# Performance work log

Measured on AMD Instinct MI355X. Metric: run time of the kernel, lower is better.

Reference implementation:

```python
import jax, jax.numpy as jnp
import numpy as np

T, B, C, H, W = 9, 8, 256, 56, 56


def setup_inputs() -> dict:
    key = jax.random.key(0)
    k1, k2, k3, k4 = jax.random.split(key, 4)
    feature_maps_sequence = jax.random.normal(k1, (T, B, C, H, W), dtype=jnp.float32)
    # Conv2d(2C, 1, kernel_size=1): weight [1, 2C, 1, 1], bias [1]
    w = jax.random.normal(k2, (1, 2 * C, 1, 1), dtype=jnp.float32) * 0.02
    b = jax.random.normal(k3, (1,), dtype=jnp.float32) * 0.02
    gamma = jax.random.normal(k4, (1,), dtype=jnp.float32)
    return {"feature_maps_sequence": feature_maps_sequence, "w": w, "b": b, "gamma": gamma}


def reference(feature_maps_sequence, w, b, gamma):
    seq = feature_maps_sequence  # [T, B, C, H, W]
    t = seq.shape[0]
    center = seq[t // 2]  # [B, C, H, W]
    c = seq.shape[2]
    # 1x1 conv over concat([center, frame]) == dot with split weight halves + bias
    w_center = w[0, :c, 0, 0]  # [C]
    w_other = w[0, c:, 0, 0]   # [C]
    score_center = jnp.einsum('bchw,c->bhw', center, w_center)          # [B, H, W]
    score_other = jnp.einsum('tbchw,c->tbhw', seq, w_other)             # [T, B, H, W]
    scores = score_center[None] + score_other + b[0]                    # [T, B, H, W]
    attn = jax.nn.softmax(scores, axis=0)                               # softmax over T
    attended = jnp.einsum('tbhw,tbchw->bchw', attn, seq)                # [B, C, H, W]
    return center + gamma * attended
```

## Files before the change

kernel.cpp:

```cpp
#include <hip/hip_runtime.h>
#include <math.h>

#define TT 9
#define BN 8
#define CC 256
#define HW 3136
#define WIN 98
#define CENTER_T 4

#define F4OP(d, expr_x, expr_y, expr_z, expr_w) \
  d.x = expr_x; d.y = expr_y; d.z = expr_z; d.w = expr_w;

__global__ __launch_bounds__(256, 2) void online_fused_kernel(
    const float* __restrict__ seq, const float* __restrict__ w,
    const float* __restrict__ gamma, float* __restrict__ out) {
  int blk = blockIdx.x;
  int b = blk / WIN;
  int win = blk - b * WIN;
  int px0 = win * 32;
  int tid = threadIdx.x;
  int wv = tid >> 6;
  int l = tid & 63;
  int quad = l & 7;
  int chg = l >> 3;
  int slot = wv * 8 + chg;
  int c0 = slot * 8;
  int px = px0 + quad * 4;

  __shared__ float4 red[TT][4][8];

  float4 wa = *(const float4*)(w + CC + c0);
  float4 wb = *(const float4*)(w + CC + c0 + 4);
  float wk[8] = {wa.x, wa.y, wa.z, wa.w, wb.x, wb.y, wb.z, wb.w};

  float4 m4 = {-1e30f, -1e30f, -1e30f, -1e30f};
  float4 s4 = {0.f, 0.f, 0.f, 0.f};
  float4 acc[8], cen[8];
  #pragma unroll
  for (int k = 0; k < 8; ++k) acc[k] = {0.f, 0.f, 0.f, 0.f};
  #pragma unroll
  for (int k = 0; k < 8; ++k) cen[k] = {0.f, 0.f, 0.f, 0.f};

  #pragma unroll
  for (int t = 0; t < TT; ++t) {
    const float* bp = seq + (((size_t)t * BN + b) * CC + c0) * HW + px;
    float4 v[8];
    #pragma unroll
    for (int k = 0; k < 8; ++k) v[k] = *(const float4*)(bp + (size_t)k * HW);

    float4 p = {0.f, 0.f, 0.f, 0.f};
    #pragma unroll
    for (int k = 0; k < 8; ++k) {
      p.x = fmaf(wk[k], v[k].x, p.x);
      p.y = fmaf(wk[k], v[k].y, p.y);
      p.z = fmaf(wk[k], v[k].z, p.z);
      p.w = fmaf(wk[k], v[k].w, p.w);
    }
    #pragma unroll
    for (int mask = 8; mask <= 32; mask <<= 1) {
      p.x += __shfl_xor(p.x, mask, 64);
      p.y += __shfl_xor(p.y, mask, 64);
      p.z += __shfl_xor(p.z, mask, 64);
      p.w += __shfl_xor(p.w, mask, 64);
    }
    if (chg == 0) red[t][wv][quad] = p;
    __syncthreads();
    float4 r0 = red[t][0][quad], r1 = red[t][1][quad];
    float4 r2 = red[t][2][quad], r3 = red[t][3][quad];
    float4 sc;
    F4OP(sc, r0.x + r1.x + r2.x + r3.x, r0.y + r1.y + r2.y + r3.y,
             r0.z + r1.z + r2.z + r3.z, r0.w + r1.w + r2.w + r3.w)

    float4 mn;
    F4OP(mn, fmaxf(m4.x, sc.x), fmaxf(m4.y, sc.y),
             fmaxf(m4.z, sc.z), fmaxf(m4.w, sc.w))
    float4 al;
    F4OP(al, __expf(m4.x - mn.x), __expf(m4.y - mn.y),
             __expf(m4.z - mn.z), __expf(m4.w - mn.w))
    float4 e;
    F4OP(e, __expf(sc.x - mn.x), __expf(sc.y - mn.y),
            __expf(sc.z - mn.z), __expf(sc.w - mn.w))
    F4OP(s4, fmaf(s4.x, al.x, e.x), fmaf(s4.y, al.y, e.y),
             fmaf(s4.z, al.z, e.z), fmaf(s4.w, al.w, e.w))
    m4 = mn;
    #pragma unroll
    for (int k = 0; k < 8; ++k) {
      acc[k].x = fmaf(acc[k].x, al.x, e.x * v[k].x);
      acc[k].y = fmaf(acc[k].y, al.y, e.y * v[k].y);
      acc[k].z = fmaf(acc[k].z, al.z, e.z * v[k].z);
      acc[k].w = fmaf(acc[k].w, al.w, e.w * v[k].w);
    }
    if (t == CENTER_T) {
      #pragma unroll
      for (int k = 0; k < 8; ++k) cen[k] = v[k];
    }
  }

  float gm = gamma[0];
  float4 gi;
  F4OP(gi, gm / s4.x, gm / s4.y, gm / s4.z, gm / s4.w)
  float* ob = out + ((size_t)b * CC + c0) * HW + px;
  #pragma unroll
  for (int k = 0; k < 8; ++k) {
    float4 o;
    o.x = fmaf(gi.x, acc[k].x, cen[k].x);
    o.y = fmaf(gi.y, acc[k].y, cen[k].y);
    o.z = fmaf(gi.z, acc[k].z, cen[k].z);
    o.w = fmaf(gi.w, acc[k].w, cen[k].w);
    *(float4*)(ob + (size_t)k * HW) = o;
  }
}

extern "C" void kernel_launch(void* const* d_in, const int* in_sizes, int n_in,
                              void* d_out, int out_size, void* d_ws, size_t ws_size,
                              hipStream_t stream) {
  const float* seq = (const float*)d_in[0];
  const float* w = (const float*)d_in[1];
  const float* gamma = (const float*)d_in[3];
  float* out = (float*)d_out;

  online_fused_kernel<<<BN * WIN, 256, 0, stream>>>(seq, w, gamma, out);
}
```

Baseline: 379.8 us.

## Split online softmax into score pass and weighted re-read pass

Replaces the per-timestep online softmax (one block barrier per frame) with a first pass that computes all nine frame scores and syncs once. A regular softmax follows, and a second pass re-reads the frames to accumulate weighted sums. The center-frame residual is folded into the attention coefficients, so the center values no longer need to be held. This removes the serialized barriers and rescaling work and lets loads issue without waiting on them, at the cost of reading the input twice and relying on cache for the second read.

```diff
diff --git a/kernel.cpp b/kernel.cpp
--- a/kernel.cpp
+++ b/kernel.cpp
@@ -8,10 +8,7 @@
 #define WIN 98
 #define CENTER_T 4
 
-#define F4OP(d, expr_x, expr_y, expr_z, expr_w) \
-  d.x = expr_x; d.y = expr_y; d.z = expr_z; d.w = expr_w;
-
-__global__ __launch_bounds__(256, 2) void online_fused_kernel(
+__global__ __launch_bounds__(256) void two_phase_kernel(
     const float* __restrict__ seq, const float* __restrict__ w,
     const float* __restrict__ gamma, float* __restrict__ out) {
   int blk = blockIdx.x;
@@ -23,8 +20,7 @@
   int l = tid & 63;
   int quad = l & 7;
   int chg = l >> 3;
-  int slot = wv * 8 + chg;
-  int c0 = slot * 8;
+  int c0 = (wv * 8 + chg) * 8;
   int px = px0 + quad * 4;
 
   __shared__ float4 red[TT][4][8];
@@ -33,28 +29,20 @@
   float4 wb = *(const float4*)(w + CC + c0 + 4);
   float wk[8] = {wa.x, wa.y, wa.z, wa.w, wb.x, wb.y, wb.z, wb.w};
 
-  float4 m4 = {-1e30f, -1e30f, -1e30f, -1e30f};
-  float4 s4 = {0.f, 0.f, 0.f, 0.f};
-  float4 acc[8], cen[8];
-  #pragma unroll
-  for (int k = 0; k < 8; ++k) acc[k] = {0.f, 0.f, 0.f, 0.f};
-  #pragma unroll
-  for (int k = 0; k < 8; ++k) cen[k] = {0.f, 0.f, 0.f, 0.f};
+  const size_t tstride = (size_t)BN * CC * HW;
+  const float* bp0 = seq + ((size_t)b * CC + c0) * HW + px;
 
   #pragma unroll
   for (int t = 0; t < TT; ++t) {
-    const float* bp = seq + (((size_t)t * BN + b) * CC + c0) * HW + px;
-    float4 v[8];
-    #pragma unroll
-    for (int k = 0; k < 8; ++k) v[k] = *(const float4*)(bp + (size_t)k * HW);
-
+    const float* bp = bp0 + t * tstride;
     float4 p = {0.f, 0.f, 0.f, 0.f};
     #pragma unroll
     for (int k = 0; k < 8; ++k) {
-      p.x = fmaf(wk[k], v[k].x, p.x);
-      p.y = fmaf(wk[k], v[k].y, p.y);
-      p.z = fmaf(wk[k], v[k].z, p.z);
-      p.w = fmaf(wk[k], v[k].w, p.w);
+      float4 v = *(const float4*)(bp + (size_t)k * HW);
+      p.x = fmaf(wk[k], v.x, p.x);
+      p.y = fmaf(wk[k], v.y, p.y);
+      p.z = fmaf(wk[k], v.z, p.z);
+      p.w = fmaf(wk[k], v.w, p.w);
     }
     #pragma unroll
     for (int mask = 8; mask <= 32; mask <<= 1) {
@@ -64,51 +52,65 @@
       p.w += __shfl_xor(p.w, mask, 64);
     }
     if (chg == 0) red[t][wv][quad] = p;
-    __syncthreads();
+  }
+  __syncthreads();
+
+  float4 ct[TT];
+  float4 m4 = {-1e30f, -1e30f, -1e30f, -1e30f};
+  #pragma unroll
+  for (int t = 0; t < TT; ++t) {
     float4 r0 = red[t][0][quad], r1 = red[t][1][quad];
     float4 r2 = red[t][2][quad], r3 = red[t][3][quad];
-    float4 sc;
-    F4OP(sc, r0.x + r1.x + r2.x + r3.x, r0.y + r1.y + r2.y + r3.y,
-             r0.z + r1.z + r2.z + r3.z, r0.w + r1.w + r2.w + r3.w)
+    float4 s;
+    s.x = r0.x + r1.x + r2.x + r3.x;
+    s.y = r0.y + r1.y + r2.y + r3.y;
+    s.z = r0.z + r1.z + r2.z + r3.z;
+    s.w = r0.w + r1.w + r2.w + r3.w;
+    ct[t] = s;
+    m4.x = fmaxf(m4.x, s.x);
+    m4.y = fmaxf(m4.y, s.y);
+    m4.z = fmaxf(m4.z, s.z);
+    m4.w = fmaxf(m4.w, s.w);
+  }
+  float4 s4 = {0.f, 0.f, 0.f, 0.f};
+  #pragma unroll
+  for (int t = 0; t < TT; ++t) {
+    ct[t].x = __expf(ct[t].x - m4.x); s4.x += ct[t].x;
+    ct[t].y = __expf(ct[t].y - m4.y); s4.y += ct[t].y;
+    ct[t].z = __expf(ct[t].z - m4.z); s4.z += ct[t].z;
+    ct[t].w = __expf(ct[t].w - m4.w); s4.w += ct[t].w;
+  }
+  float gm = gamma[0];
+  float4 gi = {gm / s4.x, gm / s4.y, gm / s4.z, gm / s4.w};
+  #pragma unroll
+  for (int t = 0; t < TT; ++t) {
+    float add = (t == CENTER_T) ? 1.f : 0.f;
+    ct[t].x = fmaf(gi.x, ct[t].x, add);
+    ct[t].y = fmaf(gi.y, ct[t].y, add);
+    ct[t].z = fmaf(gi.z, ct[t].z, add);
+    ct[t].w = fmaf(gi.w, ct[t].w, add);
+  }
 
-    float4 mn;
-    F4OP(mn, fmaxf(m4.x, sc.x), fmaxf(m4.y, sc.y),
-             fmaxf(m4.z, sc.z), fmaxf(m4.w, sc.w))
-    float4 al;
-    F4OP(al, __expf(m4.x - mn.x), __expf(m4.y - mn.y),
-             __expf(m4.z - mn.z), __expf(m4.w - mn.w))
-    float4 e;
-    F4OP(e, __expf(sc.x - mn.x), __expf(sc.y - mn.y),
-            __expf(sc.z - mn.z), __expf(sc.w - mn.w))
-    F4OP(s4, fmaf(s4.x, al.x, e.x), fmaf(s4.y, al.y, e.y),
-             fmaf(s4.z, al.z, e.z), fmaf(s4.w, al.w, e.w))
-    m4 = mn;
+  float4 acc[8];
+  #pragma unroll
+  for (int k = 0; k < 8; ++k) acc[k] = {0.f, 0.f, 0.f, 0.f};
+  #pragma unroll
+  for (int t = 0; t < TT; ++t) {
+    const float* bp = bp0 + t * tstride;
+    float4 a = ct[t];
     #pragma unroll
     for (int k = 0; k < 8; ++k) {
-      acc[k].x = fmaf(acc[k].x, al.x, e.x * v[k].x);
-      acc[k].y = fmaf(acc[k].y, al.y, e.y * v[k].y);
-      acc[k].z = fmaf(acc[k].z, al.z, e.z * v[k].z);
-      acc[k].w = fmaf(acc[k].w, al.w, e.w * v[k].w);
-    }
-    if (t == CENTER_T) {
-      #pragma unroll
-      for (int k = 0; k < 8; ++k) cen[k] = v[k];
+      float4 v = *(const float4*)(bp + (size_t)k * HW);
+      acc[k].x = fmaf(a.x, v.x, acc[k].x);
+      acc[k].y = fmaf(a.y, v.y, acc[k].y);
+      acc[k].z = fmaf(a.z, v.z, acc[k].z);
+      acc[k].w = fmaf(a.w, v.w, acc[k].w);
     }
   }
-
-  float gm = gamma[0];
-  float4 gi;
-  F4OP(gi, gm / s4.x, gm / s4.y, gm / s4.z, gm / s4.w)
   float* ob = out + ((size_t)b * CC + c0) * HW + px;
   #pragma unroll
-  for (int k = 0; k < 8; ++k) {
-    float4 o;
-    o.x = fmaf(gi.x, acc[k].x, cen[k].x);
-    o.y = fmaf(gi.y, acc[k].y, cen[k].y);
-    o.z = fmaf(gi.z, acc[k].z, cen[k].z);
-    o.w = fmaf(gi.w, acc[k].w, cen[k].w);
-    *(float4*)(ob + (size_t)k * HW) = o;
-  }
+  for (int k = 0; k < 8; ++k)
+    *(float4*)(ob + (size_t)k * HW) = acc[k];
 }
 
 extern "C" void kernel_launch(void* const* d_in, const int* in_sizes, int n_in,
@@ -119,5 +121,5 @@
   const float* gamma = (const float*)d_in[3];
   float* out = (float*)d_out;
 
-  online_fused_kernel<<<BN * WIN, 256, 0, stream>>>(seq, w, gamma, out);
+  two_phase_kernel<<<BN * WIN, 256, 0, stream>>>(seq, w, gamma, out);
 }
```

After: 357.9 us. 5.8% less time.
